# Optimization experiments

Measured on AMD Instinct MI355X. Metric: run time of the kernel, lower is better.

Reference implementation:

```python
import jax, jax.numpy as jnp
import numpy as np

N = 50000      # nodes
E = 1600000    # edges (avg degree 32)
R = 8          # relation types
G = 64         # graphs in batch
D_IN = 128
HID = 128
CLS = 10


def setup_inputs() -> dict:
    key = jax.random.key(0)
    ks = jax.random.split(key, 12)
    s = 0.05  # weight init scale
    return {
        "x": jax.random.normal(ks[0], (N, D_IN), dtype=jnp.float32),
        "edge_index": jax.random.randint(ks[1], (2, E), 0, N, dtype=jnp.int32),
        "edge_type": jax.random.randint(ks[2], (E,), 0, R, dtype=jnp.int32),
        "batch": jnp.sort(jax.random.randint(ks[3], (N,), 0, G, dtype=jnp.int32)),
        "W1": jax.random.normal(ks[4], (R, D_IN, HID), dtype=jnp.float32) * s,
        "root1": jax.random.normal(ks[5], (D_IN, HID), dtype=jnp.float32) * s,
        "b1": jax.random.normal(ks[6], (HID,), dtype=jnp.float32) * s,
        "W2": jax.random.normal(ks[7], (R, HID, HID), dtype=jnp.float32) * s,
        "root2": jax.random.normal(ks[8], (HID, HID), dtype=jnp.float32) * s,
        "b2": jax.random.normal(ks[9], (HID,), dtype=jnp.float32) * s,
        "lin_w": jax.random.normal(ks[10], (HID, CLS), dtype=jnp.float32) * s,
        "lin_b": jax.random.normal(ks[11], (CLS,), dtype=jnp.float32) * s,
    }


def rgcn_conv(x, edge_index, edge_type, W, root, bias):
    # PyG RGCNConv (default aggr='mean'): per-relation mean of neighbor
    # features, relation-specific matmul, summed over relations, + root + bias.
    src, dst = edge_index[0], edge_index[1]
    d_in = x.shape[1]
    seg = dst * R + edge_type                      # fused (node, relation) segment id
    msg = jax.ops.segment_sum(x[src], seg, num_segments=N * R)          # [N*R, d_in]
    cnt = jax.ops.segment_sum(jnp.ones((E,), x.dtype), seg, num_segments=N * R)
    mean = (msg / jnp.maximum(cnt, 1.0)[:, None]).reshape(N, R, d_in)   # [N, R, d_in]
    return jnp.einsum('nrd,rdh->nh', mean, W) + x @ root + bias


def reference(x, edge_index, edge_type, batch, W1, root1, b1, W2, root2, b2, lin_w, lin_b):
    h = jax.nn.relu(rgcn_conv(x, edge_index, edge_type, W1, root1, b1))
    h = jax.nn.relu(rgcn_conv(h, edge_index, edge_type, W2, root2, b2))
    # global mean pool per graph
    gsum = jax.ops.segment_sum(h, batch, num_segments=G)                # [G, HID]
    gcnt = jax.ops.segment_sum(jnp.ones((N,), h.dtype), batch, num_segments=G)
    g = gsum / jnp.maximum(gcnt, 1.0)[:, None]
    return g @ lin_w + lin_b                                            # [G, CLS]
```

## Files before the change

kernel.cpp:

```cpp
#include <hip/hip_runtime.h>

#define N_NODES 50000
#define N_EDGES 1600000
#define R_REL 8
#define G_GRAPHS 64
#define D_INF 128
#define HIDF 128
#define CLSF 10

#define S_SEG (N_NODES * R_REL)
#define RZ 9
#define PCHUNK 16

#define XG 8
#define NODES_PER_G (N_NODES / XG)
#define SORT_BLKS_PER_G 256
#define SORT_GRID (XG * SORT_BLKS_PER_G)

typedef __attribute__((ext_vector_type(8))) short short8;
typedef __attribute__((ext_vector_type(4))) float floatx4;

typedef __attribute__((address_space(1))) const unsigned int guint;
typedef __attribute__((address_space(3))) unsigned int luint;
__device__ __forceinline__ void gload_lds16(const void* g, void* l) {
    __builtin_amdgcn_global_load_lds((guint*)g, (luint*)l, 16, 0, 0);
}

__device__ __forceinline__ unsigned short f2bf(float f) {
    unsigned int u = __float_as_uint(f);
    unsigned int r = (u + 0x7fffu + ((u >> 16) & 1u)) >> 16;
    return (unsigned short)r;
}
__device__ __forceinline__ float bflo(unsigned int u) { return __uint_as_float(u << 16); }
__device__ __forceinline__ float bfhi(unsigned int u) { return __uint_as_float(u & 0xffff0000u); }

__device__ __forceinline__ int ntload(const int* p) { return __builtin_nontemporal_load(p); }

__global__ void seg_kernel(const int* __restrict__ dst, const int* __restrict__ et,
                           int* __restrict__ seg) {
    int e = blockIdx.x * blockDim.x + threadIdx.x;
    if (e < N_EDGES) seg[e] = dst[e] * R_REL + et[e];
}

__global__ __launch_bounds__(256) void count_kernel(const int* __restrict__ seg,
                                                    int* __restrict__ cnt) {
    int xg = blockIdx.x & (XG - 1);
    int inner = blockIdx.x >> 3;
    int lo = xg * NODES_PER_G * R_REL, hi = lo + NODES_PER_G * R_REL;
    for (int e = inner * 256 + threadIdx.x; e < N_EDGES; e += SORT_BLKS_PER_G * 256) {
        int sg = ntload(seg + e);
        if (sg >= lo && sg < hi) atomicAdd(&cnt[sg], 1);
    }
}

#define SCAN_BLK 256
#define SCAN_ELEMS 1024
#define NB_SCAN ((S_SEG + SCAN_ELEMS - 1) / SCAN_ELEMS)

__global__ __launch_bounds__(SCAN_BLK) void scan1_kernel(const int* __restrict__ cnt,
                                                         int* __restrict__ off,
                                                         int* __restrict__ bsum) {
    __shared__ int sd[SCAN_BLK];
    int t = threadIdx.x;
    int base = blockIdx.x * SCAN_ELEMS + t * 4;
    int v[4];
    int tsum = 0;
#pragma unroll
    for (int j = 0; j < 4; j++) {
        v[j] = (base + j < S_SEG) ? cnt[base + j] : 0;
        tsum += v[j];
    }
    sd[t] = tsum;
    __syncthreads();
    for (int d = 1; d < SCAN_BLK; d <<= 1) {
        int x = (t >= d) ? sd[t - d] : 0;
        __syncthreads();
        sd[t] += x;
        __syncthreads();
    }
    int incl = sd[t];
    int run = incl - tsum;
#pragma unroll
    for (int j = 0; j < 4; j++) {
        if (base + j < S_SEG) off[base + j] = run;
        run += v[j];
    }
    if (t == SCAN_BLK - 1) bsum[blockIdx.x] = incl;
}

__global__ __launch_bounds__(512) void scan2_kernel(int* __restrict__ bsum) {
    __shared__ int sd[512];
    int t = threadIdx.x;
    int v = (t < NB_SCAN) ? bsum[t] : 0;
    sd[t] = v;
    __syncthreads();
    for (int d = 1; d < 512; d <<= 1) {
        int x = (t >= d) ? sd[t - d] : 0;
        __syncthreads();
        sd[t] += x;
        __syncthreads();
    }
    if (t < NB_SCAN) bsum[t] = sd[t] - v;
}

__global__ void absoff_kernel(int* __restrict__ off, const int* __restrict__ bsum,
                              const int* __restrict__ cnt, float* __restrict__ winv) {
    int i = blockIdx.x * blockDim.x + threadIdx.x;
    if (i < S_SEG) {
        off[i] += bsum[i >> 10];
        winv[i] = 1.0f / (float)max(cnt[i], 1);
    }
}

__global__ __launch_bounds__(256) void bin_kernel(const int* __restrict__ seg,
                                                  const int* __restrict__ src,
                                                  int* __restrict__ cursor,
                                                  int* __restrict__ esrc) {
    int xg = blockIdx.x & (XG - 1);
    int inner = blockIdx.x >> 3;
    int lo = xg * NODES_PER_G * R_REL, hi = lo + NODES_PER_G * R_REL;
    for (int e = inner * 256 + threadIdx.x; e < N_EDGES; e += SORT_BLKS_PER_G * 256) {
        int sg = ntload(seg + e);
        if (sg >= lo && sg < hi) {
            int pos = atomicAdd(&cursor[sg], 1);
            esrc[pos] = ntload(src + e);
        }
    }
}

__global__ void convx_kernel(const float* __restrict__ x, unsigned short* __restrict__ xb) {
    int idx = blockIdx.x * blockDim.x + threadIdx.x;
    if (idx < N_NODES * D_INF) xb[idx] = f2bf(x[idx]);
}

__global__ __launch_bounds__(256) void convw9_kernel(const float* __restrict__ W,
                                                     const float* __restrict__ root,
                                                     unsigned short* __restrict__ wz) {
    __shared__ float t[16][17];
    int r = blockIdx.z;
    int k0 = blockIdx.x * 16, c0 = blockIdx.y * 16;
    int tx = threadIdx.x & 15, ty = threadIdx.x >> 4;
    const float* srcp = (r < 8) ? (W + (size_t)r * 128 * 128) : root;
    t[ty][tx] = srcp[(size_t)(k0 + ty) * 128 + c0 + tx];
    __syncthreads();
    wz[(size_t)r * 16384 + (size_t)(c0 + ty) * 128 + k0 + tx] = f2bf(t[tx][ty]);
}

__global__ __launch_bounds__(256) void agg_mean(
    const unsigned short* __restrict__ hsrc,
    const int* __restrict__ esrc,
    const int* __restrict__ off,
    const float* __restrict__ winv,
    unsigned short* __restrict__ m)
{
    int sg = blockIdx.x * 16 + (threadIdx.x >> 4);
    int l = threadIdx.x & 15;
    int beg = off[sg];
    int end = (sg + 1 < S_SEG) ? off[sg + 1] : N_EDGES;
    float w = winv[sg];

    float a0 = 0.f, a1 = 0.f, a2 = 0.f, a3 = 0.f;
    float a4 = 0.f, a5 = 0.f, a6 = 0.f, a7 = 0.f;
    int e = beg;
    for (; e + 4 <= end; e += 4) {
        int s0 = esrc[e], s1 = esrc[e + 1], s2 = esrc[e + 2], s3 = esrc[e + 3];
        uint4 v0 = *(const uint4*)(hsrc + (size_t)s0 * HIDF + l * 8);
        uint4 v1 = *(const uint4*)(hsrc + (size_t)s1 * HIDF + l * 8);
        uint4 v2 = *(const uint4*)(hsrc + (size_t)s2 * HIDF + l * 8);
        uint4 v3 = *(const uint4*)(hsrc + (size_t)s3 * HIDF + l * 8);
        a0 += bflo(v0.x) + bflo(v1.x) + bflo(v2.x) + bflo(v3.x);
        a1 += bfhi(v0.x) + bfhi(v1.x) + bfhi(v2.x) + bfhi(v3.x);
        a2 += bflo(v0.y) + bflo(v1.y) + bflo(v2.y) + bflo(v3.y);
        a3 += bfhi(v0.y) + bfhi(v1.y) + bfhi(v2.y) + bfhi(v3.y);
        a4 += bflo(v0.z) + bflo(v1.z) + bflo(v2.z) + bflo(v3.z);
        a5 += bfhi(v0.z) + bfhi(v1.z) + bfhi(v2.z) + bfhi(v3.z);
        a6 += bflo(v0.w) + bflo(v1.w) + bflo(v2.w) + bflo(v3.w);
        a7 += bfhi(v0.w) + bfhi(v1.w) + bfhi(v2.w) + bfhi(v3.w);
    }
    for (; e < end; e++) {
        int s0 = esrc[e];
        uint4 v0 = *(const uint4*)(hsrc + (size_t)s0 * HIDF + l * 8);
        a0 += bflo(v0.x); a1 += bfhi(v0.x);
        a2 += bflo(v0.y); a3 += bfhi(v0.y);
        a4 += bflo(v0.z); a5 += bfhi(v0.z);
        a6 += bflo(v0.w); a7 += bfhi(v0.w);
    }
    uint4 o;
    o.x = (unsigned int)f2bf(a0 * w) | ((unsigned int)f2bf(a1 * w) << 16);
    o.y = (unsigned int)f2bf(a2 * w) | ((unsigned int)f2bf(a3 * w) << 16);
    o.z = (unsigned int)f2bf(a4 * w) | ((unsigned int)f2bf(a5 * w) << 16);
    o.w = (unsigned int)f2bf(a6 * w) | ((unsigned int)f2bf(a7 * w) << 16);
    *(uint4*)(m + (size_t)sg * HIDF + l * 8) = o;
}

__global__ __launch_bounds__(256) void transform9(
    const unsigned short* __restrict__ mm,
    const unsigned short* __restrict__ hsrc,
    const unsigned short* __restrict__ wz,
    const float* __restrict__ bias,
    unsigned short* __restrict__ hout)
{
    __shared__ __align__(16) unsigned short A4[4][128][32];
    __shared__ __align__(16) unsigned short B4[4][128][32];

    const int tx = threadIdx.x;
    const int wave = tx >> 6, lane = tx & 63;
    const int quad = lane >> 4, lq = lane & 15;
    const int srow = lane >> 2, sch = lane & 3;
    const int row0 = blockIdx.x * 128;

    floatx4 acc[2][8];
#pragma unroll
    for (int i = 0; i < 2; i++)
#pragma unroll
        for (int j = 0; j < 8; j++) acc[i][j] = (floatx4){0.f, 0.f, 0.f, 0.f};

    for (int r = 0; r < RZ; r++) {
#pragma unroll
        for (int kk = 0; kk < 4; kk++) {
#pragma unroll
            for (int p = 0; p < 2; p++) {
                int rr = (wave * 2 + p) * 16;
                int gr = row0 + rr + srow; if (gr >= N_NODES) gr = N_NODES - 1;
                const unsigned short* ap = (r < 8)
                    ? mm + (size_t)gr * (R_REL * HIDF) + r * HIDF
                    : hsrc + (size_t)gr * HIDF;
                gload_lds16(ap + kk * 32 + sch * 8, &A4[kk][rr][0]);
                gload_lds16(wz + ((size_t)r * 128 + rr + srow) * 128 + kk * 32 + sch * 8,
                            &B4[kk][rr][0]);
            }
        }
        __syncthreads();

#pragma unroll
        for (int kk = 0; kk < 4; kk++) {
            short8 af[2], bfr[8];
#pragma unroll
            for (int i = 0; i < 2; i++)
                af[i] = *(const short8*)(&A4[kk][wave * 32 + i * 16 + lq][quad * 8]);
#pragma unroll
            for (int j = 0; j < 8; j++)
                bfr[j] = *(const short8*)(&B4[kk][j * 16 + lq][quad * 8]);
#pragma unroll
            for (int i = 0; i < 2; i++)
#pragma unroll
                for (int j = 0; j < 8; j++)
                    acc[i][j] = __builtin_amdgcn_mfma_f32_16x16x32_bf16(af[i], bfr[j], acc[i][j], 0, 0, 0);
        }
        __syncthreads();
    }

#pragma unroll
    for (int i = 0; i < 2; i++)
#pragma unroll
        for (int j = 0; j < 8; j++) {
            int col = j * 16 + lq;
            float bv = bias[col];
#pragma unroll
            for (int rg = 0; rg < 4; rg++) {
                int row = row0 + wave * 32 + i * 16 + quad * 4 + rg;
                if (row < N_NODES)
                    hout[(size_t)row * HIDF + col] = f2bf(fmaxf(acc[i][j][rg] + bv, 0.f));
            }
        }
}

__global__ __launch_bounds__(256) void pool1_kernel(const unsigned short* __restrict__ h,
                                                    const int* __restrict__ batch,
                                                    float* __restrict__ partial) {
    int g = blockIdx.x;
    int p = blockIdx.y;
    int lo, hi;
    {
        int l = 0, r = N_NODES;
        while (l < r) { int m = (l + r) >> 1; if (batch[m] < g) l = m + 1; else r = m; }
        lo = l;
        l = lo; r = N_NODES;
        while (l < r) { int m = (l + r) >> 1; if (batch[m] < g + 1) l = m + 1; else r = m; }
        hi = l;
    }
    int t = threadIdx.x;
    int rowlane = t >> 5;
    int c4 = t & 31;
    float a0 = 0.f, a1 = 0.f, a2 = 0.f, a3 = 0.f;
    for (int n = lo + p + rowlane * PCHUNK; n < hi; n += 8 * PCHUNK) {
        uint2 v = *(const uint2*)(h + (size_t)n * HIDF + c4 * 4);
        a0 += bflo(v.x); a1 += bfhi(v.x); a2 += bflo(v.y); a3 += bfhi(v.y);
    }
    __shared__ float red[8][128];
    if (rowlane == 0) {
        red[0][c4 * 4 + 0] = a0; red[0][c4 * 4 + 1] = a1;
        red[0][c4 * 4 + 2] = a2; red[0][c4 * 4 + 3] = a3;
    }
    __syncthreads();
    for (int s = 1; s < 8; s++) {
        if (rowlane == s) {
            red[0][c4 * 4 + 0] += a0; red[0][c4 * 4 + 1] += a1;
            red[0][c4 * 4 + 2] += a2; red[0][c4 * 4 + 3] += a3;
        }
        __syncthreads();
    }
    if (t < 128) partial[((size_t)g * PCHUNK + p) * 128 + t] = red[0][t];
}

__global__ __launch_bounds__(128) void pool2_kernel(const float* __restrict__ partial,
                                                    const int* __restrict__ batch,
                                                    float* __restrict__ gmean) {
    int g = blockIdx.x;
    int lo, hi;
    {
        int l = 0, r = N_NODES;
        while (l < r) { int m = (l + r) >> 1; if (batch[m] < g) l = m + 1; else r = m; }
        lo = l;
        l = lo; r = N_NODES;
        while (l < r) { int m = (l + r) >> 1; if (batch[m] < g + 1) l = m + 1; else r = m; }
        hi = l;
    }
    int t = threadIdx.x;
    float s = 0.f;
#pragma unroll
    for (int p = 0; p < PCHUNK; p++)
        s += partial[((size_t)g * PCHUNK + p) * 128 + t];
    gmean[g * HIDF + t] = s / (float)max(hi - lo, 1);
}

__global__ void final_kernel(const float* __restrict__ gmean,
                             const float* __restrict__ lin_w,
                             const float* __restrict__ lin_b,
                             float* __restrict__ out) {
    __shared__ float gl[HIDF];
    int g = blockIdx.x;
    int hh = threadIdx.x;
    gl[hh] = gmean[g * HIDF + hh];
    __syncthreads();
    if (hh < CLSF) {
        float s = lin_b[hh];
#pragma unroll 16
        for (int d = 0; d < HIDF; d++) s += gl[d] * lin_w[d * CLSF + hh];
        out[g * CLSF + hh] = s;
    }
}

extern "C" void kernel_launch(void* const* d_in, const int* in_sizes, int n_in,
                              void* d_out, int out_size, void* d_ws, size_t ws_size,
                              hipStream_t stream) {
    const float* x     = (const float*)d_in[0];
    const int*   ei    = (const int*)d_in[1];
    const int*   et    = (const int*)d_in[2];
    const int*   batch = (const int*)d_in[3];
    const float* W1    = (const float*)d_in[4];
    const float* root1 = (const float*)d_in[5];
    const float* b1    = (const float*)d_in[6];
    const float* W2    = (const float*)d_in[7];
    const float* root2 = (const float*)d_in[8];
    const float* b2    = (const float*)d_in[9];
    const float* lin_w = (const float*)d_in[10];
    const float* lin_b = (const float*)d_in[11];
    float* out = (float*)d_out;

    const int* src = ei;
    const int* dst = ei + N_EDGES;

    char* ws = (char*)d_ws;
    unsigned short* xb  = (unsigned short*)ws; ws += (size_t)N_NODES * HIDF * 2;
    unsigned short* h1  = (unsigned short*)ws; ws += (size_t)N_NODES * HIDF * 2;
    unsigned short* h2  = (unsigned short*)ws; ws += (size_t)N_NODES * HIDF * 2;
    unsigned short* m   = (unsigned short*)ws; ws += (size_t)S_SEG * HIDF * 2;
    unsigned short* wz1 = (unsigned short*)ws; ws += (size_t)RZ * 128 * 128 * 2;
    unsigned short* wz2 = (unsigned short*)ws; ws += (size_t)RZ * 128 * 128 * 2;
    int*   seg    = (int*)ws;   ws += (size_t)N_EDGES * 4;
    int*   cnt    = (int*)ws;   ws += (size_t)S_SEG * 4;
    int*   off    = (int*)ws;   ws += (size_t)S_SEG * 4;
    int*   bsum   = (int*)ws;   ws += 512 * 4;
    int*   cursor = (int*)ws;   ws += (size_t)S_SEG * 4;
    float* winv   = (float*)ws; ws += (size_t)S_SEG * 4;
    int*   esrc   = (int*)ws;   ws += (size_t)N_EDGES * 4;
    float* partial = (float*)ws; ws += (size_t)G_GRAPHS * PCHUNK * 128 * 4;
    float* gmean  = (float*)ws; ws += (size_t)G_GRAPHS * HIDF * 4;

    hipMemsetAsync(cnt, 0, (size_t)S_SEG * 4, stream);

    seg_kernel<<<(N_EDGES + 255) / 256, 256, 0, stream>>>(dst, et, seg);
    count_kernel<<<SORT_GRID, 256, 0, stream>>>(seg, cnt);
    scan1_kernel<<<NB_SCAN, SCAN_BLK, 0, stream>>>(cnt, off, bsum);
    scan2_kernel<<<1, 512, 0, stream>>>(bsum);
    absoff_kernel<<<(S_SEG + 255) / 256, 256, 0, stream>>>(off, bsum, cnt, winv);
    hipMemcpyAsync(cursor, off, (size_t)S_SEG * 4, hipMemcpyDeviceToDevice, stream);
    bin_kernel<<<SORT_GRID, 256, 0, stream>>>(seg, src, cursor, esrc);

    convx_kernel<<<(N_NODES * D_INF + 255) / 256, 256, 0, stream>>>(x, xb);
    convw9_kernel<<<dim3(8, 8, RZ), 256, 0, stream>>>(W1, root1, wz1);
    convw9_kernel<<<dim3(8, 8, RZ), 256, 0, stream>>>(W2, root2, wz2);

    const int NGB = (N_NODES + 127) / 128;
    const int NSB = S_SEG / 16;

    agg_mean<<<NSB, 256, 0, stream>>>(xb, esrc, off, winv, m);
    transform9<<<NGB, 256, 0, stream>>>(m, xb, wz1, b1, h1);

    agg_mean<<<NSB, 256, 0, stream>>>(h1, esrc, off, winv, m);
    transform9<<<NGB, 256, 0, stream>>>(m, h1, wz2, b2, h2);

    pool1_kernel<<<dim3(G_GRAPHS, PCHUNK), 256, 0, stream>>>(h2, batch, partial);
    pool2_kernel<<<G_GRAPHS, 128, 0, stream>>>(partial, batch, gmean);
    final_kernel<<<G_GRAPHS, HIDF, 0, stream>>>(gmean, lin_w, lin_b, out);

    (void)in_sizes; (void)n_in; (void)out_size; (void)ws_size;
}
```

Measured before the change: 473.6 us.

## Fuse segment-id and counting, replace filtered binning with two-pass partition-then-scatter

Segment-id computation and per-segment counting are fused into one vectorized kernel that reads each edge once, replacing the old count pass where every block group rescanned all edges and kept only its own node range. The binning step becomes two kernels. A partition kernel buckets (segment, src) pairs into 8 coarse node-range bins using LDS counters and one global atomic per bin per wave. A scatter kernel then handles each bin's contiguous slice, so the XG-times redundant reads of seg/src go away while atomic locality per bin is kept. The cost is an extra pairs buffer (8 bytes per edge) and two more launches.

```diff
diff --git a/kernel.cpp b/kernel.cpp
--- a/kernel.cpp
+++ b/kernel.cpp
@@ -14,8 +14,8 @@
 
 #define XG 8
 #define NODES_PER_G (N_NODES / XG)
-#define SORT_BLKS_PER_G 256
-#define SORT_GRID (XG * SORT_BLKS_PER_G)
+#define SEGS_PER_G (NODES_PER_G * R_REL)
+#define SCAT_INNER 128
 
 typedef __attribute__((ext_vector_type(8))) short short8;
 typedef __attribute__((ext_vector_type(4))) float floatx4;
@@ -34,23 +34,22 @@
 __device__ __forceinline__ float bflo(unsigned int u) { return __uint_as_float(u << 16); }
 __device__ __forceinline__ float bfhi(unsigned int u) { return __uint_as_float(u & 0xffff0000u); }
 
-__device__ __forceinline__ int ntload(const int* p) { return __builtin_nontemporal_load(p); }
-
-__global__ void seg_kernel(const int* __restrict__ dst, const int* __restrict__ et,
-                           int* __restrict__ seg) {
-    int e = blockIdx.x * blockDim.x + threadIdx.x;
-    if (e < N_EDGES) seg[e] = dst[e] * R_REL + et[e];
-}
-
-__global__ __launch_bounds__(256) void count_kernel(const int* __restrict__ seg,
-                                                    int* __restrict__ cnt) {
-    int xg = blockIdx.x & (XG - 1);
-    int inner = blockIdx.x >> 3;
-    int lo = xg * NODES_PER_G * R_REL, hi = lo + NODES_PER_G * R_REL;
-    for (int e = inner * 256 + threadIdx.x; e < N_EDGES; e += SORT_BLKS_PER_G * 256) {
-        int sg = ntload(seg + e);
-        if (sg >= lo && sg < hi) atomicAdd(&cnt[sg], 1);
-    }
+__global__ __launch_bounds__(256) void countseg_kernel(const int* __restrict__ dst,
+                                                       const int* __restrict__ et,
+                                                       int* __restrict__ seg,
+                                                       int* __restrict__ cnt) {
+    int i4 = blockIdx.x * 256 + threadIdx.x;
+    if (i4 * 4 >= N_EDGES) return;
+    int4 d = ((const int4*)dst)[i4];
+    int4 t = ((const int4*)et)[i4];
+    int4 s;
+    s.x = d.x * R_REL + t.x; s.y = d.y * R_REL + t.y;
+    s.z = d.z * R_REL + t.z; s.w = d.w * R_REL + t.w;
+    ((int4*)seg)[i4] = s;
+    atomicAdd(&cnt[s.x], 1);
+    atomicAdd(&cnt[s.y], 1);
+    atomicAdd(&cnt[s.z], 1);
+    atomicAdd(&cnt[s.w], 1);
 }
 
 #define SCAN_BLK 256
@@ -112,19 +111,62 @@
     }
 }
 
-__global__ __launch_bounds__(256) void bin_kernel(const int* __restrict__ seg,
-                                                  const int* __restrict__ src,
-                                                  int* __restrict__ cursor,
-                                                  int* __restrict__ esrc) {
+__global__ void binit_kernel(const int* __restrict__ off, int* __restrict__ bcur) {
+    int t = threadIdx.x;
+    if (t < XG) bcur[t] = off[t * SEGS_PER_G];
+}
+
+__global__ __launch_bounds__(256) void part_kernel(const int* __restrict__ seg,
+                                                   const int* __restrict__ src,
+                                                   int* __restrict__ bcur,
+                                                   int2* __restrict__ pairs) {
+    __shared__ int lcnt[4][8], lbase[4][8], lpos[4][8];
+    const int t = threadIdx.x, w = t >> 6;
+    if (t < 32) { lcnt[t >> 3][t & 7] = 0; lpos[t >> 3][t & 7] = 0; }
+    __syncthreads();
+    const int base = blockIdx.x * 2048;
+    int sg[8], sr[8];
+#pragma unroll
+    for (int q = 0; q < 2; q++) {
+        int e0 = base + (q * 256 + t) * 4;
+        if (e0 < N_EDGES) {
+            int4 s4 = *(const int4*)(seg + e0);
+            int4 r4 = *(const int4*)(src + e0);
+            sg[q * 4 + 0] = s4.x; sg[q * 4 + 1] = s4.y;
+            sg[q * 4 + 2] = s4.z; sg[q * 4 + 3] = s4.w;
+            sr[q * 4 + 0] = r4.x; sr[q * 4 + 1] = r4.y;
+            sr[q * 4 + 2] = r4.z; sr[q * 4 + 3] = r4.w;
+        } else {
+            sg[q * 4 + 0] = sg[q * 4 + 1] = sg[q * 4 + 2] = sg[q * 4 + 3] = -1;
+        }
+    }
+#pragma unroll
+    for (int j = 0; j < 8; j++)
+        if (sg[j] >= 0) atomicAdd(&lcnt[w][sg[j] / SEGS_PER_G], 1);
+    __syncthreads();
+    if (t < 32) lbase[t >> 3][t & 7] = atomicAdd(&bcur[t & 7], lcnt[t >> 3][t & 7]);
+    __syncthreads();
+#pragma unroll
+    for (int j = 0; j < 8; j++)
+        if (sg[j] >= 0) {
+            int b = sg[j] / SEGS_PER_G;
+            int p = lbase[w][b] + atomicAdd(&lpos[w][b], 1);
+            pairs[p] = make_int2(sg[j], sr[j]);
+        }
+}
+
+__global__ __launch_bounds__(256) void scat_kernel(const int2* __restrict__ pairs,
+                                                   const int* __restrict__ off,
+                                                   int* __restrict__ cursor,
+                                                   int* __restrict__ esrc) {
     int xg = blockIdx.x & (XG - 1);
     int inner = blockIdx.x >> 3;
-    int lo = xg * NODES_PER_G * R_REL, hi = lo + NODES_PER_G * R_REL;
-    for (int e = inner * 256 + threadIdx.x; e < N_EDGES; e += SORT_BLKS_PER_G * 256) {
-        int sg = ntload(seg + e);
-        if (sg >= lo && sg < hi) {
-            int pos = atomicAdd(&cursor[sg], 1);
-            esrc[pos] = ntload(src + e);
-        }
+    int bbeg = off[xg * SEGS_PER_G];
+    int bend = (xg == XG - 1) ? N_EDGES : off[(xg + 1) * SEGS_PER_G];
+    for (int i = bbeg + inner * 256 + threadIdx.x; i < bend; i += SCAT_INNER * 256) {
+        int2 pr = pairs[i];
+        int pos = atomicAdd(&cursor[pr.x], 1);
+        esrc[pos] = pr.y;
     }
 }
 
@@ -375,18 +417,21 @@
     int*   cursor = (int*)ws;   ws += (size_t)S_SEG * 4;
     float* winv   = (float*)ws; ws += (size_t)S_SEG * 4;
     int*   esrc   = (int*)ws;   ws += (size_t)N_EDGES * 4;
+    int2*  pairs  = (int2*)ws;  ws += (size_t)N_EDGES * 8;
+    int*   bcur   = (int*)ws;   ws += 64 * 4;
     float* partial = (float*)ws; ws += (size_t)G_GRAPHS * PCHUNK * 128 * 4;
     float* gmean  = (float*)ws; ws += (size_t)G_GRAPHS * HIDF * 4;
 
     hipMemsetAsync(cnt, 0, (size_t)S_SEG * 4, stream);
 
-    seg_kernel<<<(N_EDGES + 255) / 256, 256, 0, stream>>>(dst, et, seg);
-    count_kernel<<<SORT_GRID, 256, 0, stream>>>(seg, cnt);
+    countseg_kernel<<<(N_EDGES / 4 + 255) / 256, 256, 0, stream>>>(dst, et, seg, cnt);
     scan1_kernel<<<NB_SCAN, SCAN_BLK, 0, stream>>>(cnt, off, bsum);
     scan2_kernel<<<1, 512, 0, stream>>>(bsum);
     absoff_kernel<<<(S_SEG + 255) / 256, 256, 0, stream>>>(off, bsum, cnt, winv);
+    binit_kernel<<<1, 64, 0, stream>>>(off, bcur);
     hipMemcpyAsync(cursor, off, (size_t)S_SEG * 4, hipMemcpyDeviceToDevice, stream);
-    bin_kernel<<<SORT_GRID, 256, 0, stream>>>(seg, src, cursor, esrc);
+    part_kernel<<<(N_EDGES + 2047) / 2048, 256, 0, stream>>>(seg, src, bcur, pairs);
+    scat_kernel<<<XG * SCAT_INNER, 256, 0, stream>>>(pairs, off, cursor, esrc);
 
     convx_kernel<<<(N_NODES * D_INF + 255) / 256, 256, 0, stream>>>(x, xb);
     convw9_kernel<<<dim3(8, 8, RZ), 256, 0, stream>>>(W1, root1, wz1);
```

After: 516.4 us. +9.0%, slower.
